# Kernel tuning notes

Measured on AMD Instinct MI355X. Metric: run time of the kernel, lower is better.

Reference implementation:

```python
import jax, jax.numpy as jnp
import numpy as np

N, E, M = 4096, 65536, 16   # nodes, edges, channel multiplicity per degree
MID = 32                    # RadialFunc hidden width (SE3-Transformer default)
EPS = 1e-5                  # BatchNorm1d eps
DEGS = [0, 1]
PAIRS = [(0, 0), (0, 1), (1, 0), (1, 1)]  # (d_in, d_out)


def _bn_relu(x, g, b):
    # BatchNorm1d in training mode (biased batch stats over edges) + ReLU
    mu = x.mean(0, keepdims=True)
    var = ((x - mu) ** 2).mean(0, keepdims=True)
    return jax.nn.relu((x - mu) / jnp.sqrt(var + EPS) * g + b)


def _radial(feat, w1, b1, g1, be1, w2, b2, g2, be2, w3, b3, nf):
    # RadialFunc: Linear-BN-ReLU, Linear-BN-ReLU, Linear -> [E, nc_out, 1, nc_in, 1, nf]
    y = _bn_relu(feat @ w1 + b1, g1, be1)
    y = _bn_relu(y @ w2 + b2, g2, be2)
    y = y @ w3 + b3
    return y.reshape(-1, M, 1, M, 1, nf)


def _forward(h0, h1, r, basis00, basis01, basis10, basis11,
             rw1, rb1, rg1, rbe1, rw2, rb2, rg2, rbe2,
             w3_00, b3_00, w3_01, b3_01, w3_10, b3_10, w3_11, b3_11,
             Wself0, Wself1, edge_src, edge_dst):
    h = {0: h0, 1: h1}
    basis = {(0, 0): basis00, (0, 1): basis01, (1, 0): basis10, (1, 1): basis11}
    w3b3 = {(0, 0): (w3_00, b3_00), (0, 1): (w3_01, b3_01),
            (1, 0): (w3_10, b3_10), (1, 1): (w3_11, b3_11)}
    Wself = {0: Wself0, 1: Wself1}
    # PairwiseConv: per-edge kernel = sum_f R * basis  -> [E, M, 2do+1, M, 2di+1]
    kern = {}
    for p, (di, do) in enumerate(PAIRS):
        nf = 2 * min(di, do) + 1
        w3, b3 = w3b3[(di, do)]
        R = _radial(r, rw1[p], rb1[p], rg1[p], rbe1[p],
                    rw2[p], rb2[p], rg2[p], rbe2[p], w3, b3, nf)
        kern[(di, do)] = (R * basis[(di, do)]).sum(-1)
    cnt = jnp.maximum(
        jax.ops.segment_sum(jnp.ones((E,), h0.dtype), edge_dst, num_segments=N), 1.0)
    outs = []
    for do in DEGS:
        msg = jnp.zeros((E, M, 2 * do + 1), h0.dtype)
        for di in DEGS:
            # per-edge small matmul: kernel @ gathered source feature
            msg = msg + jnp.einsum('eopiq,eiq->eop', kern[(di, do)], h[di][edge_src])
        # self-interaction, flavor='skip': add W @ destination feature per edge
        msg = msg + jnp.einsum('mi,eip->emp', Wself[do][0], h[do][edge_dst])
        s = jax.ops.segment_sum(msg, edge_dst, num_segments=N)  # scatter-mean
        outs.append(s / cnt[:, None, None])
    return tuple(outs)


def setup_inputs() -> dict:
    key = jax.random.key(0)
    ks = jax.random.split(key, 20)
    nrm = lambda k, sh, s=1.0: jax.random.normal(k, sh, jnp.float32) * s
    return {
        'h0': nrm(ks[0], (N, M, 1)),
        'h1': nrm(ks[1], (N, M, 3)),
        'r': jax.random.uniform(ks[2], (E, 1), jnp.float32),
        'basis00': nrm(ks[3], (E, 1, 1, 1, 1, 1)),
        'basis01': nrm(ks[4], (E, 1, 3, 1, 1, 1)),
        'basis10': nrm(ks[5], (E, 1, 1, 1, 3, 1)),
        'basis11': nrm(ks[6], (E, 1, 3, 1, 3, 3)),
        'rw1': nrm(ks[7], (4, 1, MID)),
        'rb1': jnp.zeros((4, MID), jnp.float32),
        'rg1': jnp.ones((4, MID), jnp.float32),
        'rbe1': jnp.zeros((4, MID), jnp.float32),
        'rw2': nrm(ks[8], (4, MID, MID), 1.0 / np.sqrt(MID)),
        'rb2': jnp.zeros((4, MID), jnp.float32),
        'rg2': jnp.ones((4, MID), jnp.float32),
        'rbe2': jnp.zeros((4, MID), jnp.float32),
        'w3_00': nrm(ks[9], (MID, M * M), 1.0 / np.sqrt(MID)),
        'b3_00': jnp.zeros((M * M,), jnp.float32),
        'w3_01': nrm(ks[10], (MID, M * M), 1.0 / np.sqrt(MID)),
        'b3_01': jnp.zeros((M * M,), jnp.float32),
        'w3_10': nrm(ks[11], (MID, M * M), 1.0 / np.sqrt(MID)),
        'b3_10': jnp.zeros((M * M,), jnp.float32),
        'w3_11': nrm(ks[12], (MID, M * M * 3), 1.0 / np.sqrt(MID)),
        'b3_11': jnp.zeros((M * M * 3,), jnp.float32),
        'Wself0': nrm(ks[13], (1, M, M), 1.0 / np.sqrt(M)),
        'Wself1': nrm(ks[14], (1, M, M), 1.0 / np.sqrt(M)),
        'edge_src': jax.random.randint(ks[15], (E,), 0, N),
        'edge_dst': jax.random.randint(ks[16], (E,), 0, N),
    }


def reference(h0, h1, r, basis00, basis01, basis10, basis11,
              rw1, rb1, rg1, rbe1, rw2, rb2, rg2, rbe2,
              w3_00, b3_00, w3_01, b3_01, w3_10, b3_10, w3_11, b3_11,
              Wself0, Wself1, edge_src, edge_dst):
    return _forward(h0, h1, r, basis00, basis01, basis10, basis11,
                    rw1, rb1, rg1, rbe1, rw2, rb2, rg2, rbe2,
                    w3_00, b3_00, w3_01, b3_01, w3_10, b3_10, w3_11, b3_11,
                    Wself0, Wself1, edge_src, edge_dst)
```

## Files before the change

### kernel.cpp

```cpp
#include <hip/hip_runtime.h>

#define N_NODES 4096
#define N_EDGES 65536
#define MID 32
#define BN_EPS 1e-5f

#define WS_RSUM    0
#define WS_RSUMSQ  1
#define WS_ALPHA1  272
#define WS_BETA1   400
#define WS_A2      528
#define WS_S2      656
#define WS_GRAM    5120
#define WS_SUMY    9216
#define WS_W2T     17664
#define WS_MSG_F   262144
#define WS_U00     4456448
#define WS_U01     4521984
#define WS_V10     4587520
#define WS_W11     4784128
#define WS_DEG_I   1024
#define WS_CUR_I   9344
#define WS_OFFS_I  13440
#define WS_ELIST_I 65536
#define WSB_WA     524288
#define WSB_WB     557056
#define WSB_WC     573440

typedef short bf16x8 __attribute__((ext_vector_type(8)));
typedef float f32x4  __attribute__((ext_vector_type(4)));

__device__ __forceinline__ unsigned short f2bf(float x) {
    unsigned u = __float_as_uint(x);
    u += 0x7fffu + ((u >> 16) & 1u);
    return (unsigned short)(u >> 16);
}

__global__ void __launch_bounds__(256) k_pre(const float* __restrict__ rw2,
        const float* __restrict__ w300, const float* __restrict__ w301,
        const float* __restrict__ w310, const float* __restrict__ w311,
        const float* __restrict__ bw300, const float* __restrict__ bw301,
        const float* __restrict__ bw310, const float* __restrict__ bw311,
        const float* __restrict__ r, const int* __restrict__ edst,
        const float* __restrict__ h0, const float* __restrict__ h1,
        float* __restrict__ wsf) {
    if (blockIdx.x < 128) {
        int t = blockIdx.x * 256 + threadIdx.x;
        char* wsb = (char*)wsf;
        if (t < 4096) {
            int p = t >> 10, rem = t & 1023, c = rem >> 5, k = rem & 31;
            wsf[WS_W2T + t] = rw2[(p << 10) + (k << 5) + c];
        }
        if (t < 16384) {
            int col = t >> 5, k = t & 31;
            float v = (col < 256) ? w300[(k << 8) + col] : w310[(k << 8) + (col - 256)];
            ((unsigned short*)(wsb + WSB_WA))[t] = f2bf(v);
        }
        if (t < 8192) {
            int col = t >> 5, k = t & 31;
            ((unsigned short*)(wsb + WSB_WB))[t] = f2bf(w301[(k << 8) + col]);
        }
        if (t < 24576) {
            int col = t >> 5, k = t & 31;
            int f = col >> 8, rem = col & 255;
            ((unsigned short*)(wsb + WSB_WC))[t] = f2bf(w311[k * 768 + rem * 3 + f]);
        }
    } else if (blockIdx.x < 384) {
        int e = (blockIdx.x - 128) * 256 + threadIdx.x;
        float v = r[e];
        atomicAdd(((int*)wsf) + WS_DEG_I + edst[e], 1);
        float s = v, ss = v * v;
#pragma unroll
        for (int mk = 32; mk >= 1; mk >>= 1) {
            s  += __shfl_xor(s,  mk, 64);
            ss += __shfl_xor(ss, mk, 64);
        }
        __shared__ float ls[4], lss[4];
        int lane = threadIdx.x & 63, wv = threadIdx.x >> 6;
        if (lane == 0) { ls[wv] = s; lss[wv] = ss; }
        __syncthreads();
        if (threadIdx.x == 0) {
            atomicAdd(wsf + WS_RSUM,   ls[0] + ls[1] + ls[2] + ls[3]);
            atomicAdd(wsf + WS_RSUMSQ, lss[0] + lss[1] + lss[2] + lss[3]);
        }
    } else {
        int g = (blockIdx.x - 384) * 256 + threadIdx.x;
        int n = g >> 4, mo = g & 15;
        float h1r[48];
#pragma unroll
        for (int j = 0; j < 48; ++j) h1r[j] = h1[n * 48 + j];
        float s00 = 0.f, s01 = 0.f;
#pragma unroll
        for (int mi = 0; mi < 16; ++mi) {
            float hv = h0[n * 16 + mi];
            s00 += bw300[mo * 16 + mi] * hv;
            s01 += bw301[mo * 16 + mi] * hv;
        }
        wsf[WS_U00 + n * 16 + mo] = s00;
        wsf[WS_U01 + n * 16 + mo] = s01;
#pragma unroll
        for (int q = 0; q < 3; ++q) {
            float sv = 0.f;
#pragma unroll
            for (int mi = 0; mi < 16; ++mi)
                sv += bw310[mo * 16 + mi] * h1r[mi * 3 + q];
            wsf[WS_V10 + n * 48 + q * 16 + mo] = sv;
        }
#pragma unroll
        for (int f = 0; f < 3; ++f)
#pragma unroll
            for (int q = 0; q < 3; ++q) {
                float sv = 0.f;
#pragma unroll
                for (int mi = 0; mi < 16; ++mi)
                    sv += bw311[(mo * 16 + mi) * 3 + f] * h1r[mi * 3 + q];
                wsf[WS_W11 + n * 144 + (f * 3 + q) * 16 + mo] = sv;
            }
    }
}

__global__ void __launch_bounds__(512) k_gram(const float* __restrict__ r,
        const float* __restrict__ rw1, const float* __restrict__ rg1,
        const float* __restrict__ rbe1, float* __restrict__ wsf) {
    int t = threadIdx.x;
    int wv = t >> 6, lane = t & 63;
    int quad = lane >> 4, lq = lane & 15;
    int p  = __builtin_amdgcn_readfirstlane(wv & 3);
    int mt = __builtin_amdgcn_readfirstlane(wv >> 2);
    float mu_r  = wsf[WS_RSUM] * (1.f / N_EDGES);
    float var_r = wsf[WS_RSUMSQ] * (1.f / N_EDGES) - mu_r * mu_r;
    float al[2], be[2];
#pragma unroll
    for (int hh = 0; hh < 2; ++hh) {
        int ch = p * 32 + hh * 16 + lq;
        float w1 = rw1[ch];
        float a = w1 * rg1[ch] * rsqrtf(w1 * w1 * var_r + BN_EPS);
        al[hh] = a;
        be[hh] = rbe1[ch] - a * mu_r;
    }
    bf16x8 ones;
#pragma unroll
    for (int j = 0; j < 8; ++j) ones[j] = (short)0x3F80;
    f32x4 accG0 = {0.f, 0.f, 0.f, 0.f};
    f32x4 accG1 = {0.f, 0.f, 0.f, 0.f};
    f32x4 accS  = {0.f, 0.f, 0.f, 0.f};
    int ebase = blockIdx.x * 512;
#pragma unroll 1
    for (int ks = 0; ks < 16; ++ks) {
        const float* rp = r + ebase + ks * 32 + quad * 8;
        float4 ra = *(const float4*)(rp);
        float4 rb = *(const float4*)(rp + 4);
        float rv[8] = {ra.x, ra.y, ra.z, ra.w, rb.x, rb.y, rb.z, rb.w};
        bf16x8 fr0, fr1;
#pragma unroll
        for (int j = 0; j < 8; ++j) {
            fr0[j] = (short)f2bf(fmaxf(0.f, al[0] * rv[j] + be[0]));
            fr1[j] = (short)f2bf(fmaxf(0.f, al[1] * rv[j] + be[1]));
        }
        bf16x8 fA = mt ? fr1 : fr0;
        accG0 = __builtin_amdgcn_mfma_f32_16x16x32_bf16(fA, fr0, accG0, 0, 0, 0);
        accG1 = __builtin_amdgcn_mfma_f32_16x16x32_bf16(fA, fr1, accG1, 0, 0, 0);
        accS  = __builtin_amdgcn_mfma_f32_16x16x32_bf16(fA, ones, accS,  0, 0, 0);
    }
    float* G = wsf + WS_GRAM + p * 1024;
#pragma unroll
    for (int reg = 0; reg < 4; ++reg) {
        int k1 = mt * 16 + quad * 4 + reg;
        atomicAdd(&G[k1 * 32 + lq],      accG0[reg]);
        atomicAdd(&G[k1 * 32 + 16 + lq], accG1[reg]);
    }
    if (lq == 0) {
#pragma unroll
        for (int reg = 0; reg < 4; ++reg)
            atomicAdd(wsf + WS_SUMY + p * 32 + mt * 16 + quad * 4 + reg, accS[reg]);
    }
}

__global__ void __launch_bounds__(1024) k_fs(const float* __restrict__ rw1,
        const float* __restrict__ rg1, const float* __restrict__ rbe1,
        const float* __restrict__ rg2, const float* __restrict__ rbe2,
        const float* __restrict__ rb2, float* __restrict__ wsf) {
    int t = threadIdx.x;
    if (t < 128) {
        float mu_r  = wsf[WS_RSUM] * (1.f / N_EDGES);
        float var_r = wsf[WS_RSUMSQ] * (1.f / N_EDGES) - mu_r * mu_r;
        float w1 = rw1[t];
        float al = w1 * rg1[t] * rsqrtf(w1 * w1 * var_r + BN_EPS);
        wsf[WS_ALPHA1 + t] = al;
        wsf[WS_BETA1  + t] = rbe1[t] - al * mu_r;
        int p = t >> 5, c = t & 31;
        const float* G = wsf + WS_GRAM + p * 1024;
        const float* w = wsf + WS_W2T + p * 1024 + c * 32;
        float invE = 1.f / N_EDGES;
        float s1 = 0.f;
#pragma unroll 1
        for (int k = 0; k < 32; ++k) s1 += w[k] * (wsf[WS_SUMY + p * 32 + k] * invE);
        float q = 0.f;
#pragma unroll 1
        for (int k1 = 0; k1 < 32; ++k1) {
            float a = 0.f;
#pragma unroll
            for (int k2 = 0; k2 < 32; ++k2) a += w[k2] * G[k1 * 32 + k2];
            q += w[k1] * a;
        }
        float var = q * invE - s1 * s1;
        float a2 = rg2[t] * rsqrtf(var + BN_EPS);
        wsf[WS_A2 + t] = a2;
        float mu2 = rb2[t] + s1;
        wsf[WS_S2 + t] = rbe2[t] - mu2 * a2;
    }
    __shared__ int sdata[1024];
    const int* deg = ((const int*)wsf) + WS_DEG_I;
    int* offs = ((int*)wsf) + WS_OFFS_I;
    int* cur  = ((int*)wsf) + WS_CUR_I;
    int v0 = deg[t * 4], v1 = deg[t * 4 + 1], v2 = deg[t * 4 + 2], v3 = deg[t * 4 + 3];
    sdata[t] = v0 + v1 + v2 + v3;
    __syncthreads();
    for (int off = 1; off < 1024; off <<= 1) {
        int x = sdata[t];
        int y = (t >= off) ? sdata[t - off] : 0;
        __syncthreads();
        sdata[t] = x + y;
        __syncthreads();
    }
    int excl = (t == 0) ? 0 : sdata[t - 1];
    int o0 = excl, o1 = excl + v0, o2 = o1 + v1, o3 = o2 + v2;
    offs[t * 4] = o0;     cur[t * 4] = o0;
    offs[t * 4 + 1] = o1; cur[t * 4 + 1] = o1;
    offs[t * 4 + 2] = o2; cur[t * 4 + 2] = o2;
    offs[t * 4 + 3] = o3; cur[t * 4 + 3] = o3;
    if (t == 1023) offs[4096] = sdata[1023];
}

__global__ void __launch_bounds__(256) k_cb(const int* __restrict__ edst,
        const float* __restrict__ b00, const float* __restrict__ b01,
        const float* __restrict__ b10, const float* __restrict__ b11,
        const int* __restrict__ esrc, float* __restrict__ wsf,
        float* __restrict__ msg) {
    if (blockIdx.x < 256) {
        int e = blockIdx.x * 256 + threadIdx.x;
        int d = edst[e];
        int* cur   = ((int*)wsf) + WS_CUR_I;
        int* elist = ((int*)wsf) + WS_ELIST_I;
        int pos = atomicAdd(&cur[d], 1);
        elist[pos] = e;
        return;
    }
    int g = (blockIdx.x - 256) * 256 + threadIdx.x;
    int e = g >> 2, quad = g & 3;
    int s = esrc[e];
    float4 u00q = *(const float4*)(wsf + WS_U00 + s * 16 + quad * 4);
    float b00v = b00[e];
    float m0[4];
#pragma unroll
    for (int rr = 0; rr < 4; ++rr) m0[rr] = b00v * ((const float*)&u00q)[rr];
#pragma unroll
    for (int q = 0; q < 3; ++q) {
        float4 vq = *(const float4*)(wsf + WS_V10 + s * 48 + q * 16 + quad * 4);
        float bq = b10[e * 3 + q];
#pragma unroll
        for (int rr = 0; rr < 4; ++rr) m0[rr] += bq * ((const float*)&vq)[rr];
    }
    {
        float4 w = {m0[0], m0[1], m0[2], m0[3]};
        *(float4*)(msg + (size_t)e * 64 + quad * 4) = w;
    }
    float4 u01q = *(const float4*)(wsf + WS_U01 + s * 16 + quad * 4);
    float bo0 = b01[e * 3 + 0], bo1 = b01[e * 3 + 1], bo2 = b01[e * 3 + 2];
    float m1[4][3];
#pragma unroll
    for (int rr = 0; rr < 4; ++rr) {
        float u = ((const float*)&u01q)[rr];
        m1[rr][0] = bo0 * u; m1[rr][1] = bo1 * u; m1[rr][2] = bo2 * u;
    }
#pragma unroll
    for (int f = 0; f < 3; ++f)
#pragma unroll
        for (int q = 0; q < 3; ++q) {
            float4 wq = *(const float4*)(wsf + WS_W11 + s * 144 + (f * 3 + q) * 16 + quad * 4);
#pragma unroll
            for (int o = 0; o < 3; ++o) {
                float bas = b11[e * 27 + o * 9 + q * 3 + f];
#pragma unroll
                for (int rr = 0; rr < 4; ++rr) m1[rr][o] += bas * ((const float*)&wq)[rr];
            }
        }
    float* base = msg + (size_t)e * 64 + 16 + quad * 12;
    float4 w0 = {m1[0][0], m1[0][1], m1[0][2], m1[1][0]};
    float4 w1 = {m1[1][1], m1[1][2], m1[2][0], m1[2][1]};
    float4 w2 = {m1[2][2], m1[3][0], m1[3][1], m1[3][2]};
    *(float4*)(base)     = w0;
    *(float4*)(base + 4) = w1;
    *(float4*)(base + 8) = w2;
}

__device__ __forceinline__ void y2_lds16(int p, int el, int c0, float rv,
                                         const float* __restrict__ wsf,
                                         const float* __restrict__ rb2, char* dst) {
    float y1[MID];
#pragma unroll
    for (int k = 0; k < MID; ++k)
        y1[k] = fmaxf(0.f, wsf[WS_ALPHA1 + p * 32 + k] * rv + wsf[WS_BETA1 + p * 32 + k]);
    unsigned short h[16];
#pragma unroll
    for (int cc = 0; cc < 16; ++cc) {
        int c = c0 + cc;
        float x = rb2[p * 32 + c];
#pragma unroll
        for (int k = 0; k < MID; ++k) x += y1[k] * wsf[WS_W2T + p * 1024 + c * 32 + k];
        h[cc] = f2bf(fmaxf(0.f, wsf[WS_A2 + p * 32 + c] * x + wsf[WS_S2 + p * 32 + c]));
    }
#pragma unroll
    for (int q = 0; q < 2; ++q) {
        int4 pk;
        pk.x = (int)h[q * 8 + 0] | ((int)h[q * 8 + 1] << 16);
        pk.y = (int)h[q * 8 + 2] | ((int)h[q * 8 + 3] << 16);
        pk.z = (int)h[q * 8 + 4] | ((int)h[q * 8 + 5] << 16);
        pk.w = (int)h[q * 8 + 6] | ((int)h[q * 8 + 7] << 16);
        *(int4*)(dst + el * 64 + c0 * 2 + q * 16) = pk;
    }
}

__global__ void __launch_bounds__(512, 2) k_msg(const float* __restrict__ r,
        const float* __restrict__ h0, const float* __restrict__ h1,
        const float* __restrict__ b00, const float* __restrict__ b01,
        const float* __restrict__ b10, const float* __restrict__ b11,
        const float* __restrict__ rb2,
        const int* __restrict__ esrc,
        const float* __restrict__ wsf, float* __restrict__ msg) {
    extern __shared__ char smem[];
    short* w3s = (short*)smem;
    const char* wsb = (const char*)wsf;
    int t = threadIdx.x;
    int wv = t >> 6, lane = t & 63;
    int quad = lane >> 4, lq = lane & 15;
    int eb = blockIdx.x << 8;

    {
        const float4* src = (const float4*)(wsb + WSB_WA);
        float4* dst = (float4*)smem;
#pragma unroll
        for (int i = 0; i < 4; ++i) dst[i * 512 + t] = src[i * 512 + t];
    }
    {
        int p = __builtin_amdgcn_readfirstlane((t >> 8) * 2);
        int el = t & 255;
        float rv = r[eb + el];
        char* dst = smem + 32768 + (t >> 8) * 16384;
        y2_lds16(p, el, 0, rv, wsf, rb2, dst);
        y2_lds16(p, el, 16, rv, wsf, rb2, dst);
    }
    __syncthreads();
#pragma unroll
    for (int g2 = 0; g2 < 2; ++g2) {
        int el = (wv * 2 + g2) * 16 + lq;
        int e = eb + el;
        int s = esrc[e];
        bf16x8 bf0 = *(const bf16x8*)(smem + 32768 + el * 64 + quad * 16);
        bf16x8 bf2 = *(const bf16x8*)(smem + 49152 + el * 64 + quad * 16);
        float4 h0q = *(const float4*)(h0 + s * 16 + quad * 4);
        float4 hv0 = *(const float4*)(h1 + s * 48 + quad * 12);
        float4 hv1 = *(const float4*)(h1 + s * 48 + quad * 12 + 4);
        float4 hv2 = *(const float4*)(h1 + s * 48 + quad * 12 + 8);
        float b00v = b00[e];
        float bq0 = b10[e * 3 + 0], bq1 = b10[e * 3 + 1], bq2 = b10[e * 3 + 2];
        float gq0 = bq0 * hv0.x + bq1 * hv0.y + bq2 * hv0.z;
        float gq1 = bq0 * hv0.w + bq1 * hv1.x + bq2 * hv1.y;
        float gq2 = bq0 * hv1.z + bq1 * hv1.w + bq2 * hv2.x;
        float gq3 = bq0 * hv2.y + bq1 * hv2.z + bq2 * hv2.w;
        float4 a0v = *(const float4*)(msg + (size_t)e * 64 + quad * 4);
        float a0[4] = {a0v.x, a0v.y, a0v.z, a0v.w};
#pragma unroll
        for (int m = 0; m < 16; ++m) {
            bf16x8 af = *(const bf16x8*)(w3s + (m * 16 + lq) * 32 + quad * 8);
            f32x4 dd = __builtin_amdgcn_mfma_f32_16x16x32_bf16(af, bf0, (f32x4){0.f,0.f,0.f,0.f}, 0, 0, 0);
            float partial = dd[0] * h0q.x + dd[1] * h0q.y + dd[2] * h0q.z + dd[3] * h0q.w;
            partial += __shfl_xor(partial, 16);
            partial += __shfl_xor(partial, 32);
            a0[m & 3] += (quad == (m >> 2)) ? b00v * partial : 0.f;
        }
#pragma unroll
        for (int m = 0; m < 16; ++m) {
            bf16x8 af = *(const bf16x8*)(w3s + ((256 + m * 16 + lq) << 5) + quad * 8);
            f32x4 dd = __builtin_amdgcn_mfma_f32_16x16x32_bf16(af, bf2, (f32x4){0.f,0.f,0.f,0.f}, 0, 0, 0);
            float partial = dd[0] * gq0 + dd[1] * gq1 + dd[2] * gq2 + dd[3] * gq3;
            partial += __shfl_xor(partial, 16);
            partial += __shfl_xor(partial, 32);
            a0[m & 3] += (quad == (m >> 2)) ? partial : 0.f;
        }
        float4 w = {a0[0], a0[1], a0[2], a0[3]};
        *(float4*)(msg + (size_t)e * 64 + quad * 4) = w;
    }
    __syncthreads();

    {
        const float4* src = (const float4*)(wsb + WSB_WB);
        float4* dst = (float4*)smem;
#pragma unroll
        for (int i = 0; i < 2; ++i) dst[i * 512 + t] = src[i * 512 + t];
    }
    {
        int el = t & 255, c0 = (t >> 8) * 16;
        y2_lds16(1, el, c0, r[eb + el], wsf, rb2, smem + 16384);
    }
    __syncthreads();
#pragma unroll
    for (int g2 = 0; g2 < 2; ++g2) {
        int el = (wv * 2 + g2) * 16 + lq;
        int e = eb + el;
        int s = esrc[e];
        bf16x8 bf1 = *(const bf16x8*)(smem + 16384 + el * 64 + quad * 16);
        float4 h0q = *(const float4*)(h0 + s * 16 + quad * 4);
        float d1[4] = {0.f, 0.f, 0.f, 0.f};
#pragma unroll
        for (int m = 0; m < 16; ++m) {
            bf16x8 af = *(const bf16x8*)(w3s + (m * 16 + lq) * 32 + quad * 8);
            f32x4 dd = __builtin_amdgcn_mfma_f32_16x16x32_bf16(af, bf1, (f32x4){0.f,0.f,0.f,0.f}, 0, 0, 0);
            float partial = dd[0] * h0q.x + dd[1] * h0q.y + dd[2] * h0q.z + dd[3] * h0q.w;
            partial += __shfl_xor(partial, 16);
            partial += __shfl_xor(partial, 32);
            d1[m & 3] += (quad == (m >> 2)) ? partial : 0.f;
        }
        float bo0 = b01[e * 3 + 0], bo1 = b01[e * 3 + 1], bo2 = b01[e * 3 + 2];
        float* base = msg + (size_t)e * 64 + 16 + quad * 12;
        float4 r0 = *(const float4*)(base);
        float4 r1 = *(const float4*)(base + 4);
        float4 r2 = *(const float4*)(base + 8);
        float4 w0 = {r0.x + bo0 * d1[0], r0.y + bo1 * d1[0], r0.z + bo2 * d1[0], r0.w + bo0 * d1[1]};
        float4 w1 = {r1.x + bo1 * d1[1], r1.y + bo2 * d1[1], r1.z + bo0 * d1[2], r1.w + bo1 * d1[2]};
        float4 w2 = {r2.x + bo2 * d1[2], r2.y + bo0 * d1[3], r2.z + bo1 * d1[3], r2.w + bo2 * d1[3]};
        *(float4*)(base)     = w0;
        *(float4*)(base + 4) = w1;
        *(float4*)(base + 8) = w2;
    }
    __syncthreads();

    {
        const float4* src = (const float4*)(wsb + WSB_WC);
        float4* dst = (float4*)smem;
#pragma unroll
        for (int i = 0; i < 6; ++i) dst[i * 512 + t] = src[i * 512 + t];
    }
    {
        int el = t & 255, c0 = (t >> 8) * 16;
        y2_lds16(3, el, c0, r[eb + el], wsf, rb2, smem + 49152);
    }
    __syncthreads();
#pragma unroll
    for (int g2 = 0; g2 < 2; ++g2) {
        int el = (wv * 2 + g2) * 16 + lq;
        int e = eb + el;
        int s = esrc[e];
        bf16x8 bf3 = *(const bf16x8*)(smem + 49152 + el * 64 + quad * 16);
        float4 hv0 = *(const float4*)(h1 + s * 48 + quad * 12);
        float4 hv1 = *(const float4*)(h1 + s * 48 + quad * 12 + 4);
        float4 hv2 = *(const float4*)(h1 + s * 48 + quad * 12 + 8);
        float h1v[4][3] = {{hv0.x, hv0.y, hv0.z}, {hv0.w, hv1.x, hv1.y},
                           {hv1.z, hv1.w, hv2.x}, {hv2.y, hv2.z, hv2.w}};
        float m1[4][3];
#pragma unroll
        for (int rr = 0; rr < 4; ++rr)
#pragma unroll
            for (int o = 0; o < 3; ++o) m1[rr][o] = 0.f;
#pragma unroll
        for (int f = 0; f < 3; ++f) {
            float Tf[4][3];
#pragma unroll
            for (int o = 0; o < 3; ++o) {
                float bv0 = b11[e * 27 + o * 9 + 0 + f];
                float bv1 = b11[e * 27 + o * 9 + 3 + f];
                float bv2 = b11[e * 27 + o * 9 + 6 + f];
#pragma unroll
                for (int rr = 0; rr < 4; ++rr)
                    Tf[rr][o] = h1v[rr][0] * bv0 + h1v[rr][1] * bv1 + h1v[rr][2] * bv2;
            }
#pragma unroll
            for (int m = 0; m < 16; ++m) {
                int colb = f * 256 + m * 16 + lq;
                bf16x8 af = *(const bf16x8*)(w3s + colb * 32 + quad * 8);
                f32x4 dd = __builtin_amdgcn_mfma_f32_16x16x32_bf16(af, bf3, (f32x4){0.f,0.f,0.f,0.f}, 0, 0, 0);
#pragma unroll
                for (int o = 0; o < 3; ++o) {
                    float po = dd[0] * Tf[0][o] + dd[1] * Tf[1][o] + dd[2] * Tf[2][o] + dd[3] * Tf[3][o];
                    po += __shfl_xor(po, 16);
                    po += __shfl_xor(po, 32);
                    m1[m & 3][o] += (quad == (m >> 2)) ? po : 0.f;
                }
            }
        }
        float* base = msg + (size_t)e * 64 + 16 + quad * 12;
        float4 r0 = *(const float4*)(base);
        float4 r1 = *(const float4*)(base + 4);
        float4 r2 = *(const float4*)(base + 8);
        float4 w0 = {m1[0][0] + r0.x, m1[0][1] + r0.y, m1[0][2] + r0.z, m1[1][0] + r0.w};
        float4 w1 = {m1[1][1] + r1.x, m1[1][2] + r1.y, m1[2][0] + r1.z, m1[2][1] + r1.w};
        float4 w2 = {m1[2][2] + r2.x, m1[3][0] + r2.y, m1[3][1] + r2.z, m1[3][2] + r2.w};
        *(float4*)(base)     = w0;
        *(float4*)(base + 4) = w1;
        *(float4*)(base + 8) = w2;
    }
}

__global__ void __launch_bounds__(256) k_gather(const float* __restrict__ h0,
        const float* __restrict__ h1, const float* __restrict__ Wself0,
        const float* __restrict__ Wself1, const float* __restrict__ wsf,
        float* __restrict__ out) {
    int wv = threadIdx.x >> 6, lane = threadIdx.x & 63;
    int n = blockIdx.x * 4 + wv;
    const int* offs  = ((const int*)wsf) + WS_OFFS_I;
    const int* elist = ((const int*)wsf) + WS_ELIST_I;
    const float* msg = wsf + WS_MSG_F;
    int start = offs[n], end = offs[n + 1];
    int deg = end - start;
    float acc = 0.f;
    for (int j0 = 0; j0 < deg; j0 += 64) {
        int cnt = min(64, deg - j0);
        int eidv = (j0 + lane < deg) ? elist[start + j0 + lane] : 0;
        int jj = 0;
        for (; jj + 3 < cnt; jj += 4) {
            int e0 = __shfl(eidv, jj), e1 = __shfl(eidv, jj + 1);
            int e2 = __shfl(eidv, jj + 2), e3 = __shfl(eidv, jj + 3);
            float v0 = msg[(size_t)e0 * 64 + lane];
            float v1 = msg[(size_t)e1 * 64 + lane];
            float v2 = msg[(size_t)e2 * 64 + lane];
            float v3 = msg[(size_t)e3 * 64 + lane];
            acc += (v0 + v1) + (v2 + v3);
        }
        for (; jj < cnt; ++jj) {
            int eid = __shfl(eidv, jj);
            acc += msg[(size_t)eid * 64 + lane];
        }
    }
    float self = 0.f;
    if (lane < 16) {
        int m = lane;
#pragma unroll
        for (int i = 0; i < 16; ++i) self += Wself0[m * 16 + i] * h0[n * 16 + i];
    } else {
        int idx = lane - 16; int m = idx / 3, o = idx % 3;
#pragma unroll
        for (int i = 0; i < 16; ++i) self += Wself1[m * 16 + i] * h1[n * 48 + i * 3 + o];
    }
    float c = (float)(deg > 0 ? deg : 1);
    float res = acc / c + (deg > 0 ? self : 0.f);
    if (lane < 16) out[n * 16 + lane] = res;
    else           out[65536 + n * 48 + (lane - 16)] = res;
}

extern "C" void kernel_launch(void* const* d_in, const int* in_sizes, int n_in,
                              void* d_out, int out_size, void* d_ws, size_t ws_size,
                              hipStream_t stream) {
    const float* h0   = (const float*)d_in[0];
    const float* h1   = (const float*)d_in[1];
    const float* r    = (const float*)d_in[2];
    const float* b00  = (const float*)d_in[3];
    const float* b01  = (const float*)d_in[4];
    const float* b10  = (const float*)d_in[5];
    const float* b11  = (const float*)d_in[6];
    const float* rw1  = (const float*)d_in[7];
    const float* rg1  = (const float*)d_in[9];
    const float* rbe1 = (const float*)d_in[10];
    const float* rw2  = (const float*)d_in[11];
    const float* rb2  = (const float*)d_in[12];
    const float* rg2  = (const float*)d_in[13];
    const float* rbe2 = (const float*)d_in[14];
    const float* w300 = (const float*)d_in[15];
    const float* bw300= (const float*)d_in[16];
    const float* w301 = (const float*)d_in[17];
    const float* bw301= (const float*)d_in[18];
    const float* w310 = (const float*)d_in[19];
    const float* bw310= (const float*)d_in[20];
    const float* w311 = (const float*)d_in[21];
    const float* bw311= (const float*)d_in[22];
    const float* Wself0 = (const float*)d_in[23];
    const float* Wself1 = (const float*)d_in[24];
    const int* esrc = (const int*)d_in[25];
    const int* edst = (const int*)d_in[26];
    float* out = (float*)d_out;
    float* wsf = (float*)d_ws;
    float* msg = wsf + WS_MSG_F;

    static bool attr_set = false;
    if (!attr_set) {
        hipFuncSetAttribute((const void*)k_msg,
                            hipFuncAttributeMaxDynamicSharedMemorySize, 65536);
        attr_set = true;
    }

    hipMemsetAsync(d_ws, 0, 37376, stream);

    k_pre<<<640, 256, 0, stream>>>(rw2, w300, w301, w310, w311,
                                   bw300, bw301, bw310, bw311, r, edst, h0, h1, wsf);
    k_gram<<<128, 512, 0, stream>>>(r, rw1, rg1, rbe1, wsf);
    k_fs<<<1, 1024, 0, stream>>>(rw1, rg1, rbe1, rg2, rbe2, rb2, wsf);
    k_cb<<<1280, 256, 0, stream>>>(edst, b00, b01, b10, b11, esrc, wsf, msg);
    k_msg<<<256, 512, 65536, stream>>>(r, h0, h1, b00, b01, b10, b11, rb2,
                                       esrc, wsf, msg);
    k_gather<<<1024, 256, 0, stream>>>(h0, h1, Wself0, Wself1, wsf, out);
}
```

Measured before the change: 250.6 us.

## Fuse six kernel launches into one cooperative persistent kernel with grid syncs

Merges the preprocessing, Gram, finalize/scan, combine, message and gather stages into a single cooperative kernel of 256 blocks of 512 threads. Stages are separated by grid-wide synchronisation instead of separate launches. The intent is to remove launch gaps and tail effects between the many small kernels. In exchange, every stage is forced onto the same grid shape and occupancy, with the 64KB LDS allocation and launch bound of the heaviest stage. Stages such as the single-block scan may serialize the whole grid.

New measurement: 451.6 us. +80.2%, slower.

```diff
diff --git a/kernel.cpp b/kernel.cpp
--- a/kernel.cpp
+++ b/kernel.cpp
@@ -1,4 +1,7 @@
 #include <hip/hip_runtime.h>
+#include <hip/hip_cooperative_groups.h>
+
+namespace cg = cooperative_groups;
 
 #define N_NODES 4096
 #define N_EDGES 65536
@@ -36,264 +39,6 @@
     return (unsigned short)(u >> 16);
 }
 
-__global__ void __launch_bounds__(256) k_pre(const float* __restrict__ rw2,
-        const float* __restrict__ w300, const float* __restrict__ w301,
-        const float* __restrict__ w310, const float* __restrict__ w311,
-        const float* __restrict__ bw300, const float* __restrict__ bw301,
-        const float* __restrict__ bw310, const float* __restrict__ bw311,
-        const float* __restrict__ r, const int* __restrict__ edst,
-        const float* __restrict__ h0, const float* __restrict__ h1,
-        float* __restrict__ wsf) {
-    if (blockIdx.x < 128) {
-        int t = blockIdx.x * 256 + threadIdx.x;
-        char* wsb = (char*)wsf;
-        if (t < 4096) {
-            int p = t >> 10, rem = t & 1023, c = rem >> 5, k = rem & 31;
-            wsf[WS_W2T + t] = rw2[(p << 10) + (k << 5) + c];
-        }
-        if (t < 16384) {
-            int col = t >> 5, k = t & 31;
-            float v = (col < 256) ? w300[(k << 8) + col] : w310[(k << 8) + (col - 256)];
-            ((unsigned short*)(wsb + WSB_WA))[t] = f2bf(v);
-        }
-        if (t < 8192) {
-            int col = t >> 5, k = t & 31;
-            ((unsigned short*)(wsb + WSB_WB))[t] = f2bf(w301[(k << 8) + col]);
-        }
-        if (t < 24576) {
-            int col = t >> 5, k = t & 31;
-            int f = col >> 8, rem = col & 255;
-            ((unsigned short*)(wsb + WSB_WC))[t] = f2bf(w311[k * 768 + rem * 3 + f]);
-        }
-    } else if (blockIdx.x < 384) {
-        int e = (blockIdx.x - 128) * 256 + threadIdx.x;
-        float v = r[e];
-        atomicAdd(((int*)wsf) + WS_DEG_I + edst[e], 1);
-        float s = v, ss = v * v;
-#pragma unroll
-        for (int mk = 32; mk >= 1; mk >>= 1) {
-            s  += __shfl_xor(s,  mk, 64);
-            ss += __shfl_xor(ss, mk, 64);
-        }
-        __shared__ float ls[4], lss[4];
-        int lane = threadIdx.x & 63, wv = threadIdx.x >> 6;
-        if (lane == 0) { ls[wv] = s; lss[wv] = ss; }
-        __syncthreads();
-        if (threadIdx.x == 0) {
-            atomicAdd(wsf + WS_RSUM,   ls[0] + ls[1] + ls[2] + ls[3]);
-            atomicAdd(wsf + WS_RSUMSQ, lss[0] + lss[1] + lss[2] + lss[3]);
-        }
-    } else {
-        int g = (blockIdx.x - 384) * 256 + threadIdx.x;
-        int n = g >> 4, mo = g & 15;
-        float h1r[48];
-#pragma unroll
-        for (int j = 0; j < 48; ++j) h1r[j] = h1[n * 48 + j];
-        float s00 = 0.f, s01 = 0.f;
-#pragma unroll
-        for (int mi = 0; mi < 16; ++mi) {
-            float hv = h0[n * 16 + mi];
-            s00 += bw300[mo * 16 + mi] * hv;
-            s01 += bw301[mo * 16 + mi] * hv;
-        }
-        wsf[WS_U00 + n * 16 + mo] = s00;
-        wsf[WS_U01 + n * 16 + mo] = s01;
-#pragma unroll
-        for (int q = 0; q < 3; ++q) {
-            float sv = 0.f;
-#pragma unroll
-            for (int mi = 0; mi < 16; ++mi)
-                sv += bw310[mo * 16 + mi] * h1r[mi * 3 + q];
-            wsf[WS_V10 + n * 48 + q * 16 + mo] = sv;
-        }
-#pragma unroll
-        for (int f = 0; f < 3; ++f)
-#pragma unroll
-            for (int q = 0; q < 3; ++q) {
-                float sv = 0.f;
-#pragma unroll
-                for (int mi = 0; mi < 16; ++mi)
-                    sv += bw311[(mo * 16 + mi) * 3 + f] * h1r[mi * 3 + q];
-                wsf[WS_W11 + n * 144 + (f * 3 + q) * 16 + mo] = sv;
-            }
-    }
-}
-
-__global__ void __launch_bounds__(512) k_gram(const float* __restrict__ r,
-        const float* __restrict__ rw1, const float* __restrict__ rg1,
-        const float* __restrict__ rbe1, float* __restrict__ wsf) {
-    int t = threadIdx.x;
-    int wv = t >> 6, lane = t & 63;
-    int quad = lane >> 4, lq = lane & 15;
-    int p  = __builtin_amdgcn_readfirstlane(wv & 3);
-    int mt = __builtin_amdgcn_readfirstlane(wv >> 2);
-    float mu_r  = wsf[WS_RSUM] * (1.f / N_EDGES);
-    float var_r = wsf[WS_RSUMSQ] * (1.f / N_EDGES) - mu_r * mu_r;
-    float al[2], be[2];
-#pragma unroll
-    for (int hh = 0; hh < 2; ++hh) {
-        int ch = p * 32 + hh * 16 + lq;
-        float w1 = rw1[ch];
-        float a = w1 * rg1[ch] * rsqrtf(w1 * w1 * var_r + BN_EPS);
-        al[hh] = a;
-        be[hh] = rbe1[ch] - a * mu_r;
-    }
-    bf16x8 ones;
-#pragma unroll
-    for (int j = 0; j < 8; ++j) ones[j] = (short)0x3F80;
-    f32x4 accG0 = {0.f, 0.f, 0.f, 0.f};
-    f32x4 accG1 = {0.f, 0.f, 0.f, 0.f};
-    f32x4 accS  = {0.f, 0.f, 0.f, 0.f};
-    int ebase = blockIdx.x * 512;
-#pragma unroll 1
-    for (int ks = 0; ks < 16; ++ks) {
-        const float* rp = r + ebase + ks * 32 + quad * 8;
-        float4 ra = *(const float4*)(rp);
-        float4 rb = *(const float4*)(rp + 4);
-        float rv[8] = {ra.x, ra.y, ra.z, ra.w, rb.x, rb.y, rb.z, rb.w};
-        bf16x8 fr0, fr1;
-#pragma unroll
-        for (int j = 0; j < 8; ++j) {
-            fr0[j] = (short)f2bf(fmaxf(0.f, al[0] * rv[j] + be[0]));
-            fr1[j] = (short)f2bf(fmaxf(0.f, al[1] * rv[j] + be[1]));
-        }
-        bf16x8 fA = mt ? fr1 : fr0;
-        accG0 = __builtin_amdgcn_mfma_f32_16x16x32_bf16(fA, fr0, accG0, 0, 0, 0);
-        accG1 = __builtin_amdgcn_mfma_f32_16x16x32_bf16(fA, fr1, accG1, 0, 0, 0);
-        accS  = __builtin_amdgcn_mfma_f32_16x16x32_bf16(fA, ones, accS,  0, 0, 0);
-    }
-    float* G = wsf + WS_GRAM + p * 1024;
-#pragma unroll
-    for (int reg = 0; reg < 4; ++reg) {
-        int k1 = mt * 16 + quad * 4 + reg;
-        atomicAdd(&G[k1 * 32 + lq],      accG0[reg]);
-        atomicAdd(&G[k1 * 32 + 16 + lq], accG1[reg]);
-    }
-    if (lq == 0) {
-#pragma unroll
-        for (int reg = 0; reg < 4; ++reg)
-            atomicAdd(wsf + WS_SUMY + p * 32 + mt * 16 + quad * 4 + reg, accS[reg]);
-    }
-}
-
-__global__ void __launch_bounds__(1024) k_fs(const float* __restrict__ rw1,
-        const float* __restrict__ rg1, const float* __restrict__ rbe1,
-        const float* __restrict__ rg2, const float* __restrict__ rbe2,
-        const float* __restrict__ rb2, float* __restrict__ wsf) {
-    int t = threadIdx.x;
-    if (t < 128) {
-        float mu_r  = wsf[WS_RSUM] * (1.f / N_EDGES);
-        float var_r = wsf[WS_RSUMSQ] * (1.f / N_EDGES) - mu_r * mu_r;
-        float w1 = rw1[t];
-        float al = w1 * rg1[t] * rsqrtf(w1 * w1 * var_r + BN_EPS);
-        wsf[WS_ALPHA1 + t] = al;
-        wsf[WS_BETA1  + t] = rbe1[t] - al * mu_r;
-        int p = t >> 5, c = t & 31;
-        const float* G = wsf + WS_GRAM + p * 1024;
-        const float* w = wsf + WS_W2T + p * 1024 + c * 32;
-        float invE = 1.f / N_EDGES;
-        float s1 = 0.f;
-#pragma unroll 1
-        for (int k = 0; k < 32; ++k) s1 += w[k] * (wsf[WS_SUMY + p * 32 + k] * invE);
-        float q = 0.f;
-#pragma unroll 1
-        for (int k1 = 0; k1 < 32; ++k1) {
-            float a = 0.f;
-#pragma unroll
-            for (int k2 = 0; k2 < 32; ++k2) a += w[k2] * G[k1 * 32 + k2];
-            q += w[k1] * a;
-        }
-        float var = q * invE - s1 * s1;
-        float a2 = rg2[t] * rsqrtf(var + BN_EPS);
-        wsf[WS_A2 + t] = a2;
-        float mu2 = rb2[t] + s1;
-        wsf[WS_S2 + t] = rbe2[t] - mu2 * a2;
-    }
-    __shared__ int sdata[1024];
-    const int* deg = ((const int*)wsf) + WS_DEG_I;
-    int* offs = ((int*)wsf) + WS_OFFS_I;
-    int* cur  = ((int*)wsf) + WS_CUR_I;
-    int v0 = deg[t * 4], v1 = deg[t * 4 + 1], v2 = deg[t * 4 + 2], v3 = deg[t * 4 + 3];
-    sdata[t] = v0 + v1 + v2 + v3;
-    __syncthreads();
-    for (int off = 1; off < 1024; off <<= 1) {
-        int x = sdata[t];
-        int y = (t >= off) ? sdata[t - off] : 0;
-        __syncthreads();
-        sdata[t] = x + y;
-        __syncthreads();
-    }
-    int excl = (t == 0) ? 0 : sdata[t - 1];
-    int o0 = excl, o1 = excl + v0, o2 = o1 + v1, o3 = o2 + v2;
-    offs[t * 4] = o0;     cur[t * 4] = o0;
-    offs[t * 4 + 1] = o1; cur[t * 4 + 1] = o1;
-    offs[t * 4 + 2] = o2; cur[t * 4 + 2] = o2;
-    offs[t * 4 + 3] = o3; cur[t * 4 + 3] = o3;
-    if (t == 1023) offs[4096] = sdata[1023];
-}
-
-__global__ void __launch_bounds__(256) k_cb(const int* __restrict__ edst,
-        const float* __restrict__ b00, const float* __restrict__ b01,
-        const float* __restrict__ b10, const float* __restrict__ b11,
-        const int* __restrict__ esrc, float* __restrict__ wsf,
-        float* __restrict__ msg) {
-    if (blockIdx.x < 256) {
-        int e = blockIdx.x * 256 + threadIdx.x;
-        int d = edst[e];
-        int* cur   = ((int*)wsf) + WS_CUR_I;
-        int* elist = ((int*)wsf) + WS_ELIST_I;
-        int pos = atomicAdd(&cur[d], 1);
-        elist[pos] = e;
-        return;
-    }
-    int g = (blockIdx.x - 256) * 256 + threadIdx.x;
-    int e = g >> 2, quad = g & 3;
-    int s = esrc[e];
-    float4 u00q = *(const float4*)(wsf + WS_U00 + s * 16 + quad * 4);
-    float b00v = b00[e];
-    float m0[4];
-#pragma unroll
-    for (int rr = 0; rr < 4; ++rr) m0[rr] = b00v * ((const float*)&u00q)[rr];
-#pragma unroll
-    for (int q = 0; q < 3; ++q) {
-        float4 vq = *(const float4*)(wsf + WS_V10 + s * 48 + q * 16 + quad * 4);
-        float bq = b10[e * 3 + q];
-#pragma unroll
-        for (int rr = 0; rr < 4; ++rr) m0[rr] += bq * ((const float*)&vq)[rr];
-    }
-    {
-        float4 w = {m0[0], m0[1], m0[2], m0[3]};
-        *(float4*)(msg + (size_t)e * 64 + quad * 4) = w;
-    }
-    float4 u01q = *(const float4*)(wsf + WS_U01 + s * 16 + quad * 4);
-    float bo0 = b01[e * 3 + 0], bo1 = b01[e * 3 + 1], bo2 = b01[e * 3 + 2];
-    float m1[4][3];
-#pragma unroll
-    for (int rr = 0; rr < 4; ++rr) {
-        float u = ((const float*)&u01q)[rr];
-        m1[rr][0] = bo0 * u; m1[rr][1] = bo1 * u; m1[rr][2] = bo2 * u;
-    }
-#pragma unroll
-    for (int f = 0; f < 3; ++f)
-#pragma unroll
-        for (int q = 0; q < 3; ++q) {
-            float4 wq = *(const float4*)(wsf + WS_W11 + s * 144 + (f * 3 + q) * 16 + quad * 4);
-#pragma unroll
-            for (int o = 0; o < 3; ++o) {
-                float bas = b11[e * 27 + o * 9 + q * 3 + f];
-#pragma unroll
-                for (int rr = 0; rr < 4; ++rr) m1[rr][o] += bas * ((const float*)&wq)[rr];
-            }
-        }
-    float* base = msg + (size_t)e * 64 + 16 + quad * 12;
-    float4 w0 = {m1[0][0], m1[0][1], m1[0][2], m1[1][0]};
-    float4 w1 = {m1[1][1], m1[1][2], m1[2][0], m1[2][1]};
-    float4 w2 = {m1[2][2], m1[3][0], m1[3][1], m1[3][2]};
-    *(float4*)(base)     = w0;
-    *(float4*)(base + 4) = w1;
-    *(float4*)(base + 8) = w2;
-}
-
 __device__ __forceinline__ void y2_lds16(int p, int el, int c0, float rv,
                                          const float* __restrict__ wsf,
                                          const float* __restrict__ rb2, char* dst) {
@@ -321,230 +66,479 @@
     }
 }
 
-__global__ void __launch_bounds__(512, 2) k_msg(const float* __restrict__ r,
+__global__ void __launch_bounds__(512, 2) k_all(
+        const float* __restrict__ rw2,
+        const float* __restrict__ w300, const float* __restrict__ w301,
+        const float* __restrict__ w310, const float* __restrict__ w311,
+        const float* __restrict__ bw300, const float* __restrict__ bw301,
+        const float* __restrict__ bw310, const float* __restrict__ bw311,
+        const float* __restrict__ r, const int* __restrict__ edst,
+        const int* __restrict__ esrc,
         const float* __restrict__ h0, const float* __restrict__ h1,
         const float* __restrict__ b00, const float* __restrict__ b01,
         const float* __restrict__ b10, const float* __restrict__ b11,
-        const float* __restrict__ rb2,
-        const int* __restrict__ esrc,
-        const float* __restrict__ wsf, float* __restrict__ msg) {
+        const float* __restrict__ rw1, const float* __restrict__ rg1,
+        const float* __restrict__ rbe1, const float* __restrict__ rb2,
+        const float* __restrict__ rg2, const float* __restrict__ rbe2,
+        const float* __restrict__ Wself0, const float* __restrict__ Wself1,
+        float* __restrict__ wsf, float* __restrict__ msg,
+        float* __restrict__ out) {
     extern __shared__ char smem[];
-    short* w3s = (short*)smem;
-    const char* wsb = (const char*)wsf;
-    int t = threadIdx.x;
-    int wv = t >> 6, lane = t & 63;
+    cg::grid_group grid = cg::this_grid();
+    int tid = threadIdx.x;
+    int blk = blockIdx.x;
+    int wv = tid >> 6, lane = tid & 63;
     int quad = lane >> 4, lq = lane & 15;
-    int eb = blockIdx.x << 8;
+    char* wsb = (char*)wsf;
+
+    int t512 = blk * 512 + tid;
+    if (t512 < 65536) {
+        if (t512 < 4096) {
+            int p = t512 >> 10, rem = t512 & 1023, c = rem >> 5, k = rem & 31;
+            wsf[WS_W2T + t512] = rw2[(p << 10) + (k << 5) + c];
+        }
+        if (t512 < 16384) {
+            int col = t512 >> 5, k = t512 & 31;
+            float v = (col < 256) ? w300[(k << 8) + col] : w310[(k << 8) + (col - 256)];
+            ((unsigned short*)(wsb + WSB_WA))[t512] = f2bf(v);
+        }
+        if (t512 < 8192) {
+            int col = t512 >> 5, k = t512 & 31;
+            ((unsigned short*)(wsb + WSB_WB))[t512] = f2bf(w301[(k << 8) + col]);
+        }
+        if (t512 < 24576) {
+            int col = t512 >> 5, k = t512 & 31;
+            int f = col >> 8, rem = col & 255;
+            ((unsigned short*)(wsb + WSB_WC))[t512] = f2bf(w311[k * 768 + rem * 3 + f]);
+        }
+        int n = t512 >> 4, mo = t512 & 15;
+        float h1r[48];
+#pragma unroll
+        for (int j = 0; j < 48; ++j) h1r[j] = h1[n * 48 + j];
+        float s00 = 0.f, s01 = 0.f;
+#pragma unroll
+        for (int mi = 0; mi < 16; ++mi) {
+            float hv = h0[n * 16 + mi];
+            s00 += bw300[mo * 16 + mi] * hv;
+            s01 += bw301[mo * 16 + mi] * hv;
+        }
+        wsf[WS_U00 + n * 16 + mo] = s00;
+        wsf[WS_U01 + n * 16 + mo] = s01;
+#pragma unroll
+        for (int q = 0; q < 3; ++q) {
+            float sv = 0.f;
+#pragma unroll
+            for (int mi = 0; mi < 16; ++mi)
+                sv += bw310[mo * 16 + mi] * h1r[mi * 3 + q];
+            wsf[WS_V10 + n * 48 + q * 16 + mo] = sv;
+        }
+#pragma unroll
+        for (int f = 0; f < 3; ++f)
+#pragma unroll
+            for (int q = 0; q < 3; ++q) {
+                float sv = 0.f;
+#pragma unroll
+                for (int mi = 0; mi < 16; ++mi)
+                    sv += bw311[(mo * 16 + mi) * 3 + f] * h1r[mi * 3 + q];
+                wsf[WS_W11 + n * 144 + (f * 3 + q) * 16 + mo] = sv;
+            }
+    } else {
+        int e = t512 - 65536;
+        float v = r[e];
+        atomicAdd(((int*)wsf) + WS_DEG_I + edst[e], 1);
+        float s = v, ss = v * v;
+#pragma unroll
+        for (int mk = 32; mk >= 1; mk >>= 1) {
+            s  += __shfl_xor(s,  mk, 64);
+            ss += __shfl_xor(ss, mk, 64);
+        }
+        float* ls = (float*)smem;
+        if (lane == 0) { ls[wv] = s; ls[8 + wv] = ss; }
+        __syncthreads();
+        if (tid == 0) {
+            float a = 0.f, b = 0.f;
+#pragma unroll
+            for (int i = 0; i < 8; ++i) { a += ls[i]; b += ls[8 + i]; }
+            atomicAdd(wsf + WS_RSUM, a);
+            atomicAdd(wsf + WS_RSUMSQ, b);
+        }
+    }
+    grid.sync();
 
     {
-        const float4* src = (const float4*)(wsb + WSB_WA);
-        float4* dst = (float4*)smem;
-#pragma unroll
-        for (int i = 0; i < 4; ++i) dst[i * 512 + t] = src[i * 512 + t];
-    }
-    {
-        int p = __builtin_amdgcn_readfirstlane((t >> 8) * 2);
-        int el = t & 255;
-        float rv = r[eb + el];
-        char* dst = smem + 32768 + (t >> 8) * 16384;
-        y2_lds16(p, el, 0, rv, wsf, rb2, dst);
-        y2_lds16(p, el, 16, rv, wsf, rb2, dst);
-    }
-    __syncthreads();
-#pragma unroll
-    for (int g2 = 0; g2 < 2; ++g2) {
-        int el = (wv * 2 + g2) * 16 + lq;
-        int e = eb + el;
+        int p  = __builtin_amdgcn_readfirstlane(wv & 3);
+        int mt = __builtin_amdgcn_readfirstlane(wv >> 2);
+        float mu_r  = wsf[WS_RSUM] * (1.f / N_EDGES);
+        float var_r = wsf[WS_RSUMSQ] * (1.f / N_EDGES) - mu_r * mu_r;
+        float al[2], be[2];
+#pragma unroll
+        for (int hh = 0; hh < 2; ++hh) {
+            int ch = p * 32 + hh * 16 + lq;
+            float w1 = rw1[ch];
+            float a = w1 * rg1[ch] * rsqrtf(w1 * w1 * var_r + BN_EPS);
+            al[hh] = a;
+            be[hh] = rbe1[ch] - a * mu_r;
+        }
+        bf16x8 ones;
+#pragma unroll
+        for (int j = 0; j < 8; ++j) ones[j] = (short)0x3F80;
+        f32x4 accG0 = {0.f, 0.f, 0.f, 0.f};
+        f32x4 accG1 = {0.f, 0.f, 0.f, 0.f};
+        f32x4 accS  = {0.f, 0.f, 0.f, 0.f};
+        int ebase = blk * 256;
+#pragma unroll 1
+        for (int ks = 0; ks < 8; ++ks) {
+            const float* rp = r + ebase + ks * 32 + quad * 8;
+            float4 ra = *(const float4*)(rp);
+            float4 rb = *(const float4*)(rp + 4);
+            float rv[8] = {ra.x, ra.y, ra.z, ra.w, rb.x, rb.y, rb.z, rb.w};
+            bf16x8 fr0, fr1;
+#pragma unroll
+            for (int j = 0; j < 8; ++j) {
+                fr0[j] = (short)f2bf(fmaxf(0.f, al[0] * rv[j] + be[0]));
+                fr1[j] = (short)f2bf(fmaxf(0.f, al[1] * rv[j] + be[1]));
+            }
+            bf16x8 fA = mt ? fr1 : fr0;
+            accG0 = __builtin_amdgcn_mfma_f32_16x16x32_bf16(fA, fr0, accG0, 0, 0, 0);
+            accG1 = __builtin_amdgcn_mfma_f32_16x16x32_bf16(fA, fr1, accG1, 0, 0, 0);
+            accS  = __builtin_amdgcn_mfma_f32_16x16x32_bf16(fA, ones, accS,  0, 0, 0);
+        }
+        float* G = wsf + WS_GRAM + p * 1024;
+#pragma unroll
+        for (int reg = 0; reg < 4; ++reg) {
+            int k1 = mt * 16 + quad * 4 + reg;
+            atomicAdd(&G[k1 * 32 + lq],      accG0[reg]);
+            atomicAdd(&G[k1 * 32 + 16 + lq], accG1[reg]);
+        }
+        if (lq == 0) {
+#pragma unroll
+            for (int reg = 0; reg < 4; ++reg)
+                atomicAdd(wsf + WS_SUMY + p * 32 + mt * 16 + quad * 4 + reg, accS[reg]);
+        }
+    }
+    grid.sync();
+
+    if (blk == 0) {
+        if (tid < 128) {
+            float mu_r  = wsf[WS_RSUM] * (1.f / N_EDGES);
+            float var_r = wsf[WS_RSUMSQ] * (1.f / N_EDGES) - mu_r * mu_r;
+            float w1 = rw1[tid];
+            float al = w1 * rg1[tid] * rsqrtf(w1 * w1 * var_r + BN_EPS);
+            wsf[WS_ALPHA1 + tid] = al;
+            wsf[WS_BETA1  + tid] = rbe1[tid] - al * mu_r;
+            int p = tid >> 5, c = tid & 31;
+            const float* G = wsf + WS_GRAM + p * 1024;
+            const float* w = wsf + WS_W2T + p * 1024 + c * 32;
+            float invE = 1.f / N_EDGES;
+            float s1 = 0.f;
+#pragma unroll 1
+            for (int k = 0; k < 32; ++k) s1 += w[k] * (wsf[WS_SUMY + p * 32 + k] * invE);
+            float q = 0.f;
+#pragma unroll 1
+            for (int k1 = 0; k1 < 32; ++k1) {
+                float a = 0.f;
+#pragma unroll
+                for (int k2 = 0; k2 < 32; ++k2) a += w[k2] * G[k1 * 32 + k2];
+                q += w[k1] * a;
+            }
+            float var = q * invE - s1 * s1;
+            float a2 = rg2[tid] * rsqrtf(var + BN_EPS);
+            wsf[WS_A2 + tid] = a2;
+            float mu2 = rb2[tid] + s1;
+            wsf[WS_S2 + tid] = rbe2[tid] - mu2 * a2;
+        }
+        int* sdata = (int*)smem;
+        const int* deg = ((const int*)wsf) + WS_DEG_I;
+        int* offs = ((int*)wsf) + WS_OFFS_I;
+        int* cur  = ((int*)wsf) + WS_CUR_I;
+        int base = tid * 8;
+        int v[8]; int ssum = 0;
+#pragma unroll
+        for (int j = 0; j < 8; ++j) { v[j] = deg[base + j]; ssum += v[j]; }
+        sdata[tid] = ssum;
+        __syncthreads();
+        for (int off = 1; off < 512; off <<= 1) {
+            int x = sdata[tid];
+            int y = (tid >= off) ? sdata[tid - off] : 0;
+            __syncthreads();
+            sdata[tid] = x + y;
+            __syncthreads();
+        }
+        int run = (tid == 0) ? 0 : sdata[tid - 1];
+#pragma unroll
+        for (int j = 0; j < 8; ++j) { offs[base + j] = run; cur[base + j] = run; run += v[j]; }
+        if (tid == 511) offs[4096] = sdata[511];
+    }
+    grid.sync();
+
+    if (tid < 256) {
+        int e = blk * 256 + tid;
+        int d = edst[e];
+        int pos = atomicAdd(((int*)wsf) + WS_CUR_I + d, 1);
+        (((int*)wsf) + WS_ELIST_I)[pos] = e;
+    }
+#pragma unroll 1
+    for (int it = 0; it < 2; ++it) {
+        int g = blk * 1024 + it * 512 + tid;
+        int e = g >> 2, cq = g & 3;
         int s = esrc[e];
-        bf16x8 bf0 = *(const bf16x8*)(smem + 32768 + el * 64 + quad * 16);
-        bf16x8 bf2 = *(const bf16x8*)(smem + 49152 + el * 64 + quad * 16);
-        float4 h0q = *(const float4*)(h0 + s * 16 + quad * 4);
-        float4 hv0 = *(const float4*)(h1 + s * 48 + quad * 12);
-        float4 hv1 = *(const float4*)(h1 + s * 48 + quad * 12 + 4);
-        float4 hv2 = *(const float4*)(h1 + s * 48 + quad * 12 + 8);
+        float4 u00q = *(const float4*)(wsf + WS_U00 + s * 16 + cq * 4);
         float b00v = b00[e];
-        float bq0 = b10[e * 3 + 0], bq1 = b10[e * 3 + 1], bq2 = b10[e * 3 + 2];
-        float gq0 = bq0 * hv0.x + bq1 * hv0.y + bq2 * hv0.z;
-        float gq1 = bq0 * hv0.w + bq1 * hv1.x + bq2 * hv1.y;
-        float gq2 = bq0 * hv1.z + bq1 * hv1.w + bq2 * hv2.x;
-        float gq3 = bq0 * hv2.y + bq1 * hv2.z + bq2 * hv2.w;
-        float4 a0v = *(const float4*)(msg + (size_t)e * 64 + quad * 4);
-        float a0[4] = {a0v.x, a0v.y, a0v.z, a0v.w};
-#pragma unroll
-        for (int m = 0; m < 16; ++m) {
-            bf16x8 af = *(const bf16x8*)(w3s + (m * 16 + lq) * 32 + quad * 8);
-            f32x4 dd = __builtin_amdgcn_mfma_f32_16x16x32_bf16(af, bf0, (f32x4){0.f,0.f,0.f,0.f}, 0, 0, 0);
-            float partial = dd[0] * h0q.x + dd[1] * h0q.y + dd[2] * h0q.z + dd[3] * h0q.w;
-            partial += __shfl_xor(partial, 16);
-            partial += __shfl_xor(partial, 32);
-            a0[m & 3] += (quad == (m >> 2)) ? b00v * partial : 0.f;
-        }
-#pragma unroll
-        for (int m = 0; m < 16; ++m) {
-            bf16x8 af = *(const bf16x8*)(w3s + ((256 + m * 16 + lq) << 5) + quad * 8);
-            f32x4 dd = __builtin_amdgcn_mfma_f32_16x16x32_bf16(af, bf2, (f32x4){0.f,0.f,0.f,0.f}, 0, 0, 0);
-            float partial = dd[0] * gq0 + dd[1] * gq1 + dd[2] * gq2 + dd[3] * gq3;
-            partial += __shfl_xor(partial, 16);
-            partial += __shfl_xor(partial, 32);
-            a0[m & 3] += (quad == (m >> 2)) ? partial : 0.f;
-        }
-        float4 w = {a0[0], a0[1], a0[2], a0[3]};
-        *(float4*)(msg + (size_t)e * 64 + quad * 4) = w;
-    }
-    __syncthreads();
-
-    {
-        const float4* src = (const float4*)(wsb + WSB_WB);
-        float4* dst = (float4*)smem;
-#pragma unroll
-        for (int i = 0; i < 2; ++i) dst[i * 512 + t] = src[i * 512 + t];
-    }
-    {
-        int el = t & 255, c0 = (t >> 8) * 16;
-        y2_lds16(1, el, c0, r[eb + el], wsf, rb2, smem + 16384);
-    }
-    __syncthreads();
-#pragma unroll
-    for (int g2 = 0; g2 < 2; ++g2) {
-        int el = (wv * 2 + g2) * 16 + lq;
-        int e = eb + el;
-        int s = esrc[e];
-        bf16x8 bf1 = *(const bf16x8*)(smem + 16384 + el * 64 + quad * 16);
-        float4 h0q = *(const float4*)(h0 + s * 16 + quad * 4);
-        float d1[4] = {0.f, 0.f, 0.f, 0.f};
-#pragma unroll
-        for (int m = 0; m < 16; ++m) {
-            bf16x8 af = *(const bf16x8*)(w3s + (m * 16 + lq) * 32 + quad * 8);
-            f32x4 dd = __builtin_amdgcn_mfma_f32_16x16x32_bf16(af, bf1, (f32x4){0.f,0.f,0.f,0.f}, 0, 0, 0);
-            float partial = dd[0] * h0q.x + dd[1] * h0q.y + dd[2] * h0q.z + dd[3] * h0q.w;
-            partial += __shfl_xor(partial, 16);
-            partial += __shfl_xor(partial, 32);
-            d1[m & 3] += (quad == (m >> 2)) ? partial : 0.f;
-        }
+        float m0[4];
+#pragma unroll
+        for (int rr = 0; rr < 4; ++rr) m0[rr] = b00v * ((const float*)&u00q)[rr];
+#pragma unroll
+        for (int q = 0; q < 3; ++q) {
+            float4 vq = *(const float4*)(wsf + WS_V10 + s * 48 + q * 16 + cq * 4);
+            float bq = b10[e * 3 + q];
+#pragma unroll
+            for (int rr = 0; rr < 4; ++rr) m0[rr] += bq * ((const float*)&vq)[rr];
+        }
+        {
+            float4 w = {m0[0], m0[1], m0[2], m0[3]};
+            *(float4*)(msg + (size_t)e * 64 + cq * 4) = w;
+        }
+        float4 u01q = *(const float4*)(wsf + WS_U01 + s * 16 + cq * 4);
         float bo0 = b01[e * 3 + 0], bo1 = b01[e * 3 + 1], bo2 = b01[e * 3 + 2];
-        float* base = msg + (size_t)e * 64 + 16 + quad * 12;
-        float4 r0 = *(const float4*)(base);
-        float4 r1 = *(const float4*)(base + 4);
-        float4 r2 = *(const float4*)(base + 8);
-        float4 w0 = {r0.x + bo0 * d1[0], r0.y + bo1 * d1[0], r0.z + bo2 * d1[0], r0.w + bo0 * d1[1]};
-        float4 w1 = {r1.x + bo1 * d1[1], r1.y + bo2 * d1[1], r1.z + bo0 * d1[2], r1.w + bo1 * d1[2]};
-        float4 w2 = {r2.x + bo2 * d1[2], r2.y + bo0 * d1[3], r2.z + bo1 * d1[3], r2.w + bo2 * d1[3]};
+        float m1[4][3];
+#pragma unroll
+        for (int rr = 0; rr < 4; ++rr) {
+            float u = ((const float*)&u01q)[rr];
+            m1[rr][0] = bo0 * u; m1[rr][1] = bo1 * u; m1[rr][2] = bo2 * u;
+        }
+#pragma unroll
+        for (int f = 0; f < 3; ++f)
+#pragma unroll
+            for (int q = 0; q < 3; ++q) {
+                float4 wq = *(const float4*)(wsf + WS_W11 + s * 144 + (f * 3 + q) * 16 + cq * 4);
+#pragma unroll
+                for (int o = 0; o < 3; ++o) {
+                    float bas = b11[e * 27 + o * 9 + q * 3 + f];
+#pragma unroll
+                    for (int rr = 0; rr < 4; ++rr) m1[rr][o] += bas * ((const float*)&wq)[rr];
+                }
+            }
+        float* base = msg + (size_t)e * 64 + 16 + cq * 12;
+        float4 w0 = {m1[0][0], m1[0][1], m1[0][2], m1[1][0]};
+        float4 w1 = {m1[1][1], m1[1][2], m1[2][0], m1[2][1]};
+        float4 w2 = {m1[2][2], m1[3][0], m1[3][1], m1[3][2]};
         *(float4*)(base)     = w0;
         *(float4*)(base + 4) = w1;
         *(float4*)(base + 8) = w2;
     }
-    __syncthreads();
+    grid.sync();
 
     {
-        const float4* src = (const float4*)(wsb + WSB_WC);
-        float4* dst = (float4*)smem;
-#pragma unroll
-        for (int i = 0; i < 6; ++i) dst[i * 512 + t] = src[i * 512 + t];
-    }
+        short* w3s = (short*)smem;
+        int eb = blk << 8;
+        {
+            const float4* src = (const float4*)(wsb + WSB_WA);
+            float4* dst = (float4*)smem;
+#pragma unroll
+            for (int i = 0; i < 4; ++i) dst[i * 512 + tid] = src[i * 512 + tid];
+        }
+        {
+            int p = __builtin_amdgcn_readfirstlane((tid >> 8) * 2);
+            int el = tid & 255;
+            float rv = r[eb + el];
+            char* dst = smem + 32768 + (tid >> 8) * 16384;
+            y2_lds16(p, el, 0, rv, wsf, rb2, dst);
+            y2_lds16(p, el, 16, rv, wsf, rb2, dst);
+        }
+        __syncthreads();
+#pragma unroll
+        for (int g2 = 0; g2 < 2; ++g2) {
+            int el = (wv * 2 + g2) * 16 + lq;
+            int e = eb + el;
+            int s = esrc[e];
+            bf16x8 bf0 = *(const bf16x8*)(smem + 32768 + el * 64 + quad * 16);
+            bf16x8 bf2 = *(const bf16x8*)(smem + 49152 + el * 64 + quad * 16);
+            float4 h0q = *(const float4*)(h0 + s * 16 + quad * 4);
+            float4 hv0 = *(const float4*)(h1 + s * 48 + quad * 12);
+            float4 hv1 = *(const float4*)(h1 + s * 48 + quad * 12 + 4);
+            float4 hv2 = *(const float4*)(h1 + s * 48 + quad * 12 + 8);
+            float b00v = b00[e];
+            float bq0 = b10[e * 3 + 0], bq1 = b10[e * 3 + 1], bq2 = b10[e * 3 + 2];
+            float gq0 = bq0 * hv0.x + bq1 * hv0.y + bq2 * hv0.z;
+            float gq1 = bq0 * hv0.w + bq1 * hv1.x + bq2 * hv1.y;
+            float gq2 = bq0 * hv1.z + bq1 * hv1.w + bq2 * hv2.x;
+            float gq3 = bq0 * hv2.y + bq1 * hv2.z + bq2 * hv2.w;
+            float4 a0v = *(const float4*)(msg + (size_t)e * 64 + quad * 4);
+            float a0[4] = {a0v.x, a0v.y, a0v.z, a0v.w};
+#pragma unroll
+            for (int m = 0; m < 16; ++m) {
+                bf16x8 af = *(const bf16x8*)(w3s + (m * 16 + lq) * 32 + quad * 8);
+                f32x4 dd = __builtin_amdgcn_mfma_f32_16x16x32_bf16(af, bf0, (f32x4){0.f,0.f,0.f,0.f}, 0, 0, 0);
+                float partial = dd[0] * h0q.x + dd[1] * h0q.y + dd[2] * h0q.z + dd[3] * h0q.w;
+                partial += __shfl_xor(partial, 16);
+                partial += __shfl_xor(partial, 32);
+                a0[m & 3] += (quad == (m >> 2)) ? b00v * partial : 0.f;
+            }
+#pragma unroll
+            for (int m = 0; m < 16; ++m) {
+                bf16x8 af = *(const bf16x8*)(w3s + ((256 + m * 16 + lq) << 5) + quad * 8);
+                f32x4 dd = __builtin_amdgcn_mfma_f32_16x16x32_bf16(af, bf2, (f32x4){0.f,0.f,0.f,0.f}, 0, 0, 0);
+                float partial = dd[0] * gq0 + dd[1] * gq1 + dd[2] * gq2 + dd[3] * gq3;
+                partial += __shfl_xor(partial, 16);
+                partial += __shfl_xor(partial, 32);
+                a0[m & 3] += (quad == (m >> 2)) ? partial : 0.f;
+            }
+            float4 w = {a0[0], a0[1], a0[2], a0[3]};
+            *(float4*)(msg + (size_t)e * 64 + quad * 4) = w;
+        }
+        __syncthreads();
+        {
+            const float4* src = (const float4*)(wsb + WSB_WB);
+            float4* dst = (float4*)smem;
+#pragma unroll
+            for (int i = 0; i < 2; ++i) dst[i * 512 + tid] = src[i * 512 + tid];
+        }
+        {
+            int el = tid & 255, c0 = (tid >> 8) * 16;
+            y2_lds16(1, el, c0, r[eb + el], wsf, rb2, smem + 16384);
+        }
+        __syncthreads();
+#pragma unroll
+        for (int g2 = 0; g2 < 2; ++g2) {
+            int el = (wv * 2 + g2) * 16 + lq;
+            int e = eb + el;
+            int s = esrc[e];
+            bf16x8 bf1 = *(const bf16x8*)(smem + 16384 + el * 64 + quad * 16);
+            float4 h0q = *(const float4*)(h0 + s * 16 + quad * 4);
+            float d1[4] = {0.f, 0.f, 0.f, 0.f};
+#pragma unroll
+            for (int m = 0; m < 16; ++m) {
+                bf16x8 af = *(const bf16x8*)(w3s + (m * 16 + lq) * 32 + quad * 8);
+                f32x4 dd = __builtin_amdgcn_mfma_f32_16x16x32_bf16(af, bf1, (f32x4){0.f,0.f,0.f,0.f}, 0, 0, 0);
+                float partial = dd[0] * h0q.x + dd[1] * h0q.y + dd[2] * h0q.z + dd[3] * h0q.w;
+                partial += __shfl_xor(partial, 16);
+                partial += __shfl_xor(partial, 32);
+                d1[m & 3] += (quad == (m >> 2)) ? partial : 0.f;
+            }
+            float bo0 = b01[e * 3 + 0], bo1 = b01[e * 3 + 1], bo2 = b01[e * 3 + 2];
+            float* base = msg + (size_t)e * 64 + 16 + quad * 12;
+            float4 r0 = *(const float4*)(base);
+            float4 r1 = *(const float4*)(base + 4);
+            float4 r2 = *(const float4*)(base + 8);
+            float4 w0 = {r0.x + bo0 * d1[0], r0.y + bo1 * d1[0], r0.z + bo2 * d1[0], r0.w + bo0 * d1[1]};
+            float4 w1 = {r1.x + bo1 * d1[1], r1.y + bo2 * d1[1], r1.z + bo0 * d1[2], r1.w + bo1 * d1[2]};
+            float4 w2 = {r2.x + bo2 * d1[2], r2.y + bo0 * d1[3], r2.z + bo1 * d1[3], r2.w + bo2 * d1[3]};
+            *(float4*)(base)     = w0;
+            *(float4*)(base + 4) = w1;
+            *(float4*)(base + 8) = w2;
+        }
+        __syncthreads();
+        {
+            const float4* src = (const float4*)(wsb + WSB_WC);
+            float4* dst = (float4*)smem;
+#pragma unroll
+            for (int i = 0; i < 6; ++i) dst[i * 512 + tid] = src[i * 512 + tid];
+        }
+        {
+            int el = tid & 255, c0 = (tid >> 8) * 16;
+            y2_lds16(3, el, c0, r[eb + el], wsf, rb2, smem + 49152);
+        }
+        __syncthreads();
+#pragma unroll
+        for (int g2 = 0; g2 < 2; ++g2) {
+            int el = (wv * 2 + g2) * 16 + lq;
+            int e = eb + el;
+            int s = esrc[e];
+            bf16x8 bf3 = *(const bf16x8*)(smem + 49152 + el * 64 + quad * 16);
+            float4 hv0 = *(const float4*)(h1 + s * 48 + quad * 12);
+            float4 hv1 = *(const float4*)(h1 + s * 48 + quad * 12 + 4);
+            float4 hv2 = *(const float4*)(h1 + s * 48 + quad * 12 + 8);
+            float h1v[4][3] = {{hv0.x, hv0.y, hv0.z}, {hv0.w, hv1.x, hv1.y},
+                               {hv1.z, hv1.w, hv2.x}, {hv2.y, hv2.z, hv2.w}};
+            float m1[4][3];
+#pragma unroll
+            for (int rr = 0; rr < 4; ++rr)
+#pragma unroll
+                for (int o = 0; o < 3; ++o) m1[rr][o] = 0.f;
+#pragma unroll
+            for (int f = 0; f < 3; ++f) {
+                float Tf[4][3];
+#pragma unroll
+                for (int o = 0; o < 3; ++o) {
+                    float bv0 = b11[e * 27 + o * 9 + 0 + f];
+                    float bv1 = b11[e * 27 + o * 9 + 3 + f];
+                    float bv2 = b11[e * 27 + o * 9 + 6 + f];
+#pragma unroll
+                    for (int rr = 0; rr < 4; ++rr)
+                        Tf[rr][o] = h1v[rr][0] * bv0 + h1v[rr][1] * bv1 + h1v[rr][2] * bv2;
+                }
+#pragma unroll
+                for (int m = 0; m < 16; ++m) {
+                    int colb = f * 256 + m * 16 + lq;
+                    bf16x8 af = *(const bf16x8*)(w3s + colb * 32 + quad * 8);
+                    f32x4 dd = __builtin_amdgcn_mfma_f32_16x16x32_bf16(af, bf3, (f32x4){0.f,0.f,0.f,0.f}, 0, 0, 0);
+#pragma unroll
+                    for (int o = 0; o < 3; ++o) {
+                        float po = dd[0] * Tf[0][o] + dd[1] * Tf[1][o] + dd[2] * Tf[2][o] + dd[3] * Tf[3][o];
+                        po += __shfl_xor(po, 16);
+                        po += __shfl_xor(po, 32);
+                        m1[m & 3][o] += (quad == (m >> 2)) ? po : 0.f;
+                    }
+                }
+            }
+            float* base = msg + (size_t)e * 64 + 16 + quad * 12;
+            float4 r0 = *(const float4*)(base);
+            float4 r1 = *(const float4*)(base + 4);
+            float4 r2 = *(const float4*)(base + 8);
+            float4 w0 = {m1[0][0] + r0.x, m1[0][1] + r0.y, m1[0][2] + r0.z, m1[1][0] + r0.w};
+            float4 w1 = {m1[1][1] + r1.x, m1[1][2] + r1.y, m1[2][0] + r1.z, m1[2][1] + r1.w};
+            float4 w2 = {m1[2][2] + r2.x, m1[3][0] + r2.y, m1[3][1] + r2.z, m1[3][2] + r2.w};
+            *(float4*)(base)     = w0;
+            *(float4*)(base + 4) = w1;
+            *(float4*)(base + 8) = w2;
+        }
+    }
+    grid.sync();
+
     {
-        int el = t & 255, c0 = (t >> 8) * 16;
-        y2_lds16(3, el, c0, r[eb + el], wsf, rb2, smem + 49152);
-    }
-    __syncthreads();
-#pragma unroll
-    for (int g2 = 0; g2 < 2; ++g2) {
-        int el = (wv * 2 + g2) * 16 + lq;
-        int e = eb + el;
-        int s = esrc[e];
-        bf16x8 bf3 = *(const bf16x8*)(smem + 49152 + el * 64 + quad * 16);
-        float4 hv0 = *(const float4*)(h1 + s * 48 + quad * 12);
-        float4 hv1 = *(const float4*)(h1 + s * 48 + quad * 12 + 4);
-        float4 hv2 = *(const float4*)(h1 + s * 48 + quad * 12 + 8);
-        float h1v[4][3] = {{hv0.x, hv0.y, hv0.z}, {hv0.w, hv1.x, hv1.y},
-                           {hv1.z, hv1.w, hv2.x}, {hv2.y, hv2.z, hv2.w}};
-        float m1[4][3];
-#pragma unroll
-        for (int rr = 0; rr < 4; ++rr)
-#pragma unroll
-            for (int o = 0; o < 3; ++o) m1[rr][o] = 0.f;
-#pragma unroll
-        for (int f = 0; f < 3; ++f) {
-            float Tf[4][3];
-#pragma unroll
-            for (int o = 0; o < 3; ++o) {
-                float bv0 = b11[e * 27 + o * 9 + 0 + f];
-                float bv1 = b11[e * 27 + o * 9 + 3 + f];
-                float bv2 = b11[e * 27 + o * 9 + 6 + f];
-#pragma unroll
-                for (int rr = 0; rr < 4; ++rr)
-                    Tf[rr][o] = h1v[rr][0] * bv0 + h1v[rr][1] * bv1 + h1v[rr][2] * bv2;
-            }
-#pragma unroll
-            for (int m = 0; m < 16; ++m) {
-                int colb = f * 256 + m * 16 + lq;
-                bf16x8 af = *(const bf16x8*)(w3s + colb * 32 + quad * 8);
-                f32x4 dd = __builtin_amdgcn_mfma_f32_16x16x32_bf16(af, bf3, (f32x4){0.f,0.f,0.f,0.f}, 0, 0, 0);
-#pragma unroll
-                for (int o = 0; o < 3; ++o) {
-                    float po = dd[0] * Tf[0][o] + dd[1] * Tf[1][o] + dd[2] * Tf[2][o] + dd[3] * Tf[3][o];
-                    po += __shfl_xor(po, 16);
-                    po += __shfl_xor(po, 32);
-                    m1[m & 3][o] += (quad == (m >> 2)) ? po : 0.f;
+        const int* offs  = ((const int*)wsf) + WS_OFFS_I;
+        const int* elist = ((const int*)wsf) + WS_ELIST_I;
+        const float* msgr = msg;
+#pragma unroll 1
+        for (int nn = 0; nn < 2; ++nn) {
+            int n = blk * 16 + wv * 2 + nn;
+            int start = offs[n], end = offs[n + 1];
+            int deg = end - start;
+            float acc = 0.f;
+            for (int j0 = 0; j0 < deg; j0 += 64) {
+                int cnt = min(64, deg - j0);
+                int eidv = (j0 + lane < deg) ? elist[start + j0 + lane] : 0;
+                int jj = 0;
+                for (; jj + 3 < cnt; jj += 4) {
+                    int e0 = __shfl(eidv, jj), e1 = __shfl(eidv, jj + 1);
+                    int e2 = __shfl(eidv, jj + 2), e3 = __shfl(eidv, jj + 3);
+                    float v0 = msgr[(size_t)e0 * 64 + lane];
+                    float v1 = msgr[(size_t)e1 * 64 + lane];
+                    float v2 = msgr[(size_t)e2 * 64 + lane];
+                    float v3 = msgr[(size_t)e3 * 64 + lane];
+                    acc += (v0 + v1) + (v2 + v3);
                 }
-            }
-        }
-        float* base = msg + (size_t)e * 64 + 16 + quad * 12;
-        float4 r0 = *(const float4*)(base);
-        float4 r1 = *(const float4*)(base + 4);
-        float4 r2 = *(const float4*)(base + 8);
-        float4 w0 = {m1[0][0] + r0.x, m1[0][1] + r0.y, m1[0][2] + r0.z, m1[1][0] + r0.w};
-        float4 w1 = {m1[1][1] + r1.x, m1[1][2] + r1.y, m1[2][0] + r1.z, m1[2][1] + r1.w};
-        float4 w2 = {m1[2][2] + r2.x, m1[3][0] + r2.y, m1[3][1] + r2.z, m1[3][2] + r2.w};
-        *(float4*)(base)     = w0;
-        *(float4*)(base + 4) = w1;
-        *(float4*)(base + 8) = w2;
-    }
-}
-
-__global__ void __launch_bounds__(256) k_gather(const float* __restrict__ h0,
-        const float* __restrict__ h1, const float* __restrict__ Wself0,
-        const float* __restrict__ Wself1, const float* __restrict__ wsf,
-        float* __restrict__ out) {
-    int wv = threadIdx.x >> 6, lane = threadIdx.x & 63;
-    int n = blockIdx.x * 4 + wv;
-    const int* offs  = ((const int*)wsf) + WS_OFFS_I;
-    const int* elist = ((const int*)wsf) + WS_ELIST_I;
-    const float* msg = wsf + WS_MSG_F;
-    int start = offs[n], end = offs[n + 1];
-    int deg = end - start;
-    float acc = 0.f;
-    for (int j0 = 0; j0 < deg; j0 += 64) {
-        int cnt = min(64, deg - j0);
-        int eidv = (j0 + lane < deg) ? elist[start + j0 + lane] : 0;
-        int jj = 0;
-        for (; jj + 3 < cnt; jj += 4) {
-            int e0 = __shfl(eidv, jj), e1 = __shfl(eidv, jj + 1);
-            int e2 = __shfl(eidv, jj + 2), e3 = __shfl(eidv, jj + 3);
-            float v0 = msg[(size_t)e0 * 64 + lane];
-            float v1 = msg[(size_t)e1 * 64 + lane];
-            float v2 = msg[(size_t)e2 * 64 + lane];
-            float v3 = msg[(size_t)e3 * 64 + lane];
-            acc += (v0 + v1) + (v2 + v3);
-        }
-        for (; jj < cnt; ++jj) {
-            int eid = __shfl(eidv, jj);
-            acc += msg[(size_t)eid * 64 + lane];
-        }
-    }
-    float self = 0.f;
-    if (lane < 16) {
-        int m = lane;
-#pragma unroll
-        for (int i = 0; i < 16; ++i) self += Wself0[m * 16 + i] * h0[n * 16 + i];
-    } else {
-        int idx = lane - 16; int m = idx / 3, o = idx % 3;
-#pragma unroll
-        for (int i = 0; i < 16; ++i) self += Wself1[m * 16 + i] * h1[n * 48 + i * 3 + o];
-    }
-    float c = (float)(deg > 0 ? deg : 1);
-    float res = acc / c + (deg > 0 ? self : 0.f);
-    if (lane < 16) out[n * 16 + lane] = res;
-    else           out[65536 + n * 48 + (lane - 16)] = res;
+                for (; jj < cnt; ++jj) {
+                    int eid = __shfl(eidv, jj);
+                    acc += msgr[(size_t)eid * 64 + lane];
+                }
+            }
+            float self = 0.f;
+            if (lane < 16) {
+                int m = lane;
+#pragma unroll
+                for (int i = 0; i < 16; ++i) self += Wself0[m * 16 + i] * h0[n * 16 + i];
+            } else {
+                int idx = lane - 16; int m = idx / 3, o = idx % 3;
+#pragma unroll
+                for (int i = 0; i < 16; ++i) self += Wself1[m * 16 + i] * h1[n * 48 + i * 3 + o];
+            }
+            float c = (float)(deg > 0 ? deg : 1);
+            float res = acc / c + (deg > 0 ? self : 0.f);
+            if (lane < 16) out[n * 16 + lane] = res;
+            else           out[65536 + n * 48 + (lane - 16)] = res;
+        }
+    }
 }
 
 extern "C" void kernel_launch(void* const* d_in, const int* in_sizes, int n_in,
@@ -582,19 +576,22 @@
 
     static bool attr_set = false;
     if (!attr_set) {
-        hipFuncSetAttribute((const void*)k_msg,
+        hipFuncSetAttribute((const void*)k_all,
                             hipFuncAttributeMaxDynamicSharedMemorySize, 65536);
         attr_set = true;
     }
 
     hipMemsetAsync(d_ws, 0, 37376, stream);
 
-    k_pre<<<640, 256, 0, stream>>>(rw2, w300, w301, w310, w311,
-                                   bw300, bw301, bw310, bw311, r, edst, h0, h1, wsf);
-    k_gram<<<128, 512, 0, stream>>>(r, rw1, rg1, rbe1, wsf);
-    k_fs<<<1, 1024, 0, stream>>>(rw1, rg1, rbe1, rg2, rbe2, rb2, wsf);
-    k_cb<<<1280, 256, 0, stream>>>(edst, b00, b01, b10, b11, esrc, wsf, msg);
-    k_msg<<<256, 512, 65536, stream>>>(r, h0, h1, b00, b01, b10, b11, rb2,
-                                       esrc, wsf, msg);
-    k_gather<<<1024, 256, 0, stream>>>(h0, h1, Wself0, Wself1, wsf, out);
+    void* args[] = {
+        (void*)&rw2, (void*)&w300, (void*)&w301, (void*)&w310, (void*)&w311,
+        (void*)&bw300, (void*)&bw301, (void*)&bw310, (void*)&bw311,
+        (void*)&r, (void*)&edst, (void*)&esrc, (void*)&h0, (void*)&h1,
+        (void*)&b00, (void*)&b01, (void*)&b10, (void*)&b11,
+        (void*)&rw1, (void*)&rg1, (void*)&rbe1, (void*)&rb2,
+        (void*)&rg2, (void*)&rbe2, (void*)&Wself0, (void*)&Wself1,
+        (void*)&wsf, (void*)&msg, (void*)&out
+    };
+    hipLaunchCooperativeKernel((const void*)k_all, dim3(256), dim3(512),
+                               args, 65536, stream);
 }
```
